# Kernel tuning notes

Measured on AMD Instinct MI355X. Metric: run time of the kernel, lower is better.

The kernel has to match this reference:

```python
import jax, jax.numpy as jnp
import numpy as np

INPUT_SIZE = 4
SEQ = 256
EMB = 64
QKV = 64
BATCH = 64
INDICES = np.array([0, 0, 1, 1])
BLK = SEQ // INPUT_SIZE                      # 64 positions per block
POS_GROUP = np.repeat(INDICES, BLK)          # per-position group id, shape [SEQ]
NUM_HEADS = len(np.unique(INDICES))          # 2
GROUP_POS = [np.where(POS_GROUP == g)[0] for g in range(NUM_HEADS)]  # static index sets


def _linear_params(key, din, dout):
    # torch nn.Linear default init: U(-1/sqrt(din), 1/sqrt(din))
    kw, kb = jax.random.split(key)
    s = 1.0 / np.sqrt(din)
    W = jax.random.uniform(kw, (dout, din), jnp.float32, -s, s)
    b = jax.random.uniform(kb, (dout,), jnp.float32, -s, s)
    return W, b


def setup_inputs() -> dict:
    key = jax.random.key(0)
    keys = jax.random.split(key, 1 + 3 * NUM_HEADS)
    inp = {"x": jax.random.normal(keys[0], (BATCH, SEQ, EMB), jnp.float32)}
    for g in range(NUM_HEADS):
        L = len(GROUP_POS[g])                # 128
        din, dout = L * EMB, L * QKV         # 8192 -> 8192
        WQ, bQ = _linear_params(keys[1 + 3 * g + 0], din, dout)
        WK, bK = _linear_params(keys[1 + 3 * g + 1], din, dout)
        WV, bV = _linear_params(keys[1 + 3 * g + 2], din, dout)
        inp[f"WQ{g}"], inp[f"bQ{g}"] = WQ, bQ
        inp[f"WK{g}"], inp[f"bK{g}"] = WK, bK
        inp[f"WV{g}"], inp[f"bV{g}"] = WV, bV
    return inp


def _head(xs, WQ, bQ, WK, bK, WV, bV, L):
    # xs: [B, L*EMB] flattened group slice
    B = xs.shape[0]
    Q = (xs @ WQ.T + bQ).reshape(B, L, QKV)
    K = (xs @ WK.T + bK).reshape(B, L, QKV)
    V = (xs @ WV.T + bV).reshape(B, L, QKV)
    scores = jnp.einsum("bik,bjk->bij", Q, K)        # [B, L, L]
    # Original uses nn.Softmax(dim=1): normalize over the QUERY axis (axis=1).
    attn = jax.nn.softmax(scores, axis=1)
    Z = jnp.einsum("bij,bjk->bik", attn, V)
    # coeff applied AFTER attention @ V, as in the original
    return Z * (1.0 / jnp.sqrt(jnp.float32(QKV)))


def reference(x, WQ0, bQ0, WK0, bK0, WV0, bV0, WQ1, bQ1, WK1, bK1, WV1, bV1):
    params = [(WQ0, bQ0, WK0, bK0, WV0, bV0), (WQ1, bQ1, WK1, bK1, WV1, bV1)]
    B = x.shape[0]
    out = jnp.zeros((B, SEQ, QKV), jnp.float32)
    for g in range(NUM_HEADS):                        # small static loop over groups
        pos = GROUP_POS[g]
        L = len(pos)
        xs = x[:, pos, :].reshape(B, L * EMB)
        Z = _head(xs, *params[g], L)
        out = out.at[:, pos, :].set(Z)
    return out
```

## Files before the change

kernel.cpp:

```cpp
#include <hip/hip_runtime.h>
#include <hip/hip_bf16.h>

#define BATCH 64
#define SEQ   256
#define EMB   64
#define QKVD  64
#define KD    8192
#define ND    8192
#define SEQD  16384
#define BKT   256
#define NTK   (KD / BKT)

typedef __attribute__((ext_vector_type(8))) short bf16x8;
typedef __attribute__((ext_vector_type(4))) float f32x4;

struct WArgs { const float* W[6]; const float* b[6]; };

__device__ __forceinline__ short f2bf(float f) {
    unsigned u = __builtin_bit_cast(unsigned, f);
    u += 0x7fffu + ((u >> 16) & 1u);
    return (short)(u >> 16);
}

__device__ __forceinline__ void gl16(const void* g, void* l) {
    __builtin_amdgcn_global_load_lds(
        (const __attribute__((address_space(1))) void*)g,
        (__attribute__((address_space(3))) void*)l, 16, 0, 0);
}

__device__ __forceinline__ void barrier_fenced() {
    asm volatile("" ::: "memory");
    __builtin_amdgcn_s_barrier();
    asm volatile("" ::: "memory");
}

__global__ __launch_bounds__(256)
void cvt_x_kernel(const float* __restrict__ x, short* __restrict__ xb) {
    const int i = (blockIdx.x * 256 + threadIdx.x) * 4;
    float4 v = *reinterpret_cast<const float4*>(x + i);
    short4 o;
    o.x = f2bf(v.x); o.y = f2bf(v.y); o.z = f2bf(v.z); o.w = f2bf(v.w);
    *reinterpret_cast<short4*>(xb + i) = o;
}

__global__ __launch_bounds__(256, 2)
void qkv_gemm_kernel(const short* __restrict__ xb, WArgs wa,
                     float* __restrict__ qkv) {
    __shared__ __attribute__((aligned(16))) float W_lds[2][32 * BKT];
    __shared__ __attribute__((aligned(16))) short A_lds[32 * BKT];

    const int wv  = threadIdx.x >> 6;
    const int ln  = threadIdx.x & 63;
    const int r   = ln & 15;
    const int kb  = ln >> 4;
    const int key = r & 7;
    const int mq  = wv & 1;
    const int nq  = wv >> 1;

    const int bid = blockIdx.x;
    const int xcd = bid & 7;
    const int q   = bid >> 3;
    const int mh  = q & 1;
    const int p   = xcd * 192 + (q >> 1);
    const int gi  = p >> 8;
    const int n0  = (p & 255) * 32;
    const int g   = gi / 3;
    const int m0  = mh * 32;

    const char*  __restrict__ Wb8 =
        (const char*)(wa.W[gi] + (size_t)n0 * KD);
    const short* __restrict__ Ag = xb + g * KD;

    f32x4 acc = {0.f, 0.f, 0.f, 0.f};

    auto stageW = [&](int t, int slot) {
        const char* tb = Wb8 + (size_t)t * 1024;
        #pragma unroll
        for (int i = 0; i < 8; ++i) {
            const int row = wv * 8 + i;
            gl16(tb + (size_t)row * (KD * 4) + ((ln ^ (row & 7)) << 4),
                 (char*)&W_lds[slot][0] + row * 1024);
        }
    };
    auto stageA = [&](int t) {
        #pragma unroll
        for (int j = 0; j < 4; ++j) {
            const int jj  = wv * 4 + j;
            const int row = 2 * jj + (ln >> 5);
            const int c   = (ln & 31) ^ (row & 7);
            gl16((const char*)(Ag + (size_t)(m0 + row) * SEQD)
                     + (size_t)t * 512 + (c << 4),
                 (char*)&A_lds[0] + jj * 1024);
        }
    };

    auto compute = [&](int slot) {
        const float* Wrow = &W_lds[slot][0] + (nq * 16 + r) * BKT;
        const char*  Ab   = (const char*)&A_lds[0] + (mq * 16 + r) * 512;
        #pragma unroll
        for (int s = 0; s < 8; ++s) {
            const int cg = s * 8 + kb * 2;
            f32x4 w0 = *(const f32x4*)(Wrow + (((cg)     ^ key) << 2));
            f32x4 w1 = *(const f32x4*)(Wrow + (((cg + 1) ^ key) << 2));
            bf16x8 bb;
            bb[0] = f2bf(w0[0]); bb[1] = f2bf(w0[1]);
            bb[2] = f2bf(w0[2]); bb[3] = f2bf(w0[3]);
            bb[4] = f2bf(w1[0]); bb[5] = f2bf(w1[1]);
            bb[6] = f2bf(w1[2]); bb[7] = f2bf(w1[3]);
            const int ca = (s * 4 + kb) ^ key;
            const bf16x8 a = *(const bf16x8*)(Ab + (ca << 4));
            acc = __builtin_amdgcn_mfma_f32_16x16x32_bf16(a, bb, acc, 0, 0, 0);
        }
    };

    stageW(0, 0);
    stageA(0);
    stageW(1, 1);

    for (int t = 0; t < NTK; ++t) {
        if (t < NTK - 1) { asm volatile("s_waitcnt vmcnt(8)" ::: "memory"); }
        else             { asm volatile("s_waitcnt vmcnt(0)" ::: "memory"); }
        __builtin_amdgcn_sched_barrier(0);
        barrier_fenced();
        compute(t & 1);
        barrier_fenced();
        if (t + 1 < NTK) stageA(t + 1);
        if (t + 2 < NTK) stageW(t + 2, t & 1);
    }

    const int nbr = n0 + nq * 16 + r;
    const float bias = wa.b[gi][nbr];
    float* orow = qkv + (size_t)gi * (BATCH * ND) + nbr;
    #pragma unroll
    for (int reg = 0; reg < 4; ++reg) {
        const int m = m0 + mq * 16 + kb * 4 + reg;
        orow[(size_t)m * ND] = acc[reg] + bias;
    }
}

__global__ __launch_bounds__(256)
void attn_kernel(const float* __restrict__ qkv, float* __restrict__ out) {
    __shared__ float Ql[128 * 65];
    __shared__ float Kl[128 * 65];
    __shared__ float Sc[128 * 129];
    __shared__ float Pm[256];
    __shared__ float Ps[256];
    __shared__ float Rden[128];

    const int b = blockIdx.x;
    const int g = blockIdx.y;
    const int t = threadIdx.x;

    const float* __restrict__ Qg = qkv + ((size_t)(3 * g + 0) * BATCH + b) * ND;
    const float* __restrict__ Kg = qkv + ((size_t)(3 * g + 1) * BATCH + b) * ND;
    const float* __restrict__ Vg = qkv + ((size_t)(3 * g + 2) * BATCH + b) * ND;

    for (int e = t; e < 8192; e += 256) {
        const int i = e >> 6, k = e & 63;
        Ql[i * 65 + k] = Qg[e];
        Kl[i * 65 + k] = Kg[e];
    }
    __syncthreads();

    {
        const int i0 = (t >> 4) * 8;
        const int j0 = (t & 15) * 8;
        float s[8][8];
        #pragma unroll
        for (int rr = 0; rr < 8; ++rr)
            #pragma unroll
            for (int cc = 0; cc < 8; ++cc) s[rr][cc] = 0.f;
        for (int k = 0; k < 64; ++k) {
            float qv[8], kv[8];
            #pragma unroll
            for (int rr = 0; rr < 8; ++rr) qv[rr] = Ql[(i0 + rr) * 65 + k];
            #pragma unroll
            for (int cc = 0; cc < 8; ++cc) kv[cc] = Kl[(j0 + cc) * 65 + k];
            #pragma unroll
            for (int rr = 0; rr < 8; ++rr)
                #pragma unroll
                for (int cc = 0; cc < 8; ++cc)
                    s[rr][cc] = fmaf(qv[rr], kv[cc], s[rr][cc]);
        }
        #pragma unroll
        for (int rr = 0; rr < 8; ++rr)
            #pragma unroll
            for (int cc = 0; cc < 8; ++cc)
                Sc[(i0 + rr) * 129 + (j0 + cc)] = s[rr][cc];
    }
    __syncthreads();

    const int j = t & 127, h = t >> 7;
    {
        for (int e = t; e < 8192; e += 256) {
            const int i = e >> 6, k = e & 63;
            Ql[i * 65 + k] = Vg[e];
        }
        float m = -3.0e38f;
        for (int i = h * 64; i < h * 64 + 64; ++i)
            m = fmaxf(m, Sc[i * 129 + j]);
        Pm[h * 128 + j] = m;
    }
    __syncthreads();
    {
        const float m = fmaxf(Pm[j], Pm[128 + j]);
        float sum = 0.f;
        for (int i = h * 64; i < h * 64 + 64; ++i) {
            const float e = __expf(Sc[i * 129 + j] - m);
            Sc[i * 129 + j] = e;
            sum += e;
        }
        Ps[h * 128 + j] = sum;
    }
    __syncthreads();
    if (t < 128) Rden[t] = 1.0f / (Ps[t] + Ps[128 + t]);
    __syncthreads();

    {
        const int i0 = (t >> 4) * 8;
        const int k0 = (t & 15) * 4;
        float z[8][4];
        #pragma unroll
        for (int rr = 0; rr < 8; ++rr)
            #pragma unroll
            for (int cc = 0; cc < 4; ++cc) z[rr][cc] = 0.f;
        for (int jj = 0; jj < 128; ++jj) {
            const float rd = Rden[jj];
            float av[8], vv[4];
            #pragma unroll
            for (int rr = 0; rr < 8; ++rr) av[rr] = Sc[(i0 + rr) * 129 + jj] * rd;
            #pragma unroll
            for (int cc = 0; cc < 4; ++cc) vv[cc] = Ql[jj * 65 + k0 + cc];
            #pragma unroll
            for (int rr = 0; rr < 8; ++rr)
                #pragma unroll
                for (int cc = 0; cc < 4; ++cc)
                    z[rr][cc] = fmaf(av[rr], vv[cc], z[rr][cc]);
        }
        float* op = out + (size_t)b * (SEQ * QKVD) + (size_t)(g * 128) * QKVD + k0;
        #pragma unroll
        for (int rr = 0; rr < 8; ++rr) {
            float4 o;
            o.x = z[rr][0] * 0.125f; o.y = z[rr][1] * 0.125f;
            o.z = z[rr][2] * 0.125f; o.w = z[rr][3] * 0.125f;
            *reinterpret_cast<float4*>(op + (size_t)(i0 + rr) * QKVD) = o;
        }
    }
}

extern "C" void kernel_launch(void* const* d_in, const int* in_sizes, int n_in,
                              void* d_out, int out_size, void* d_ws, size_t ws_size,
                              hipStream_t stream) {
    const float* x = (const float*)d_in[0];
    WArgs wa;
    for (int g = 0; g < 2; ++g)
        for (int q = 0; q < 3; ++q) {
            wa.W[g * 3 + q] = (const float*)d_in[1 + g * 6 + q * 2];
            wa.b[g * 3 + q] = (const float*)d_in[2 + g * 6 + q * 2];
        }

    short* xb  = (short*)d_ws;
    float* qkv = (float*)((char*)d_ws + (size_t)4 * 1024 * 1024);

    cvt_x_kernel<<<dim3(1024), dim3(256), 0, stream>>>(x, xb);
    qkv_gemm_kernel<<<dim3(3072), dim3(256), 0, stream>>>(xb, wa, qkv);
    attn_kernel<<<dim3(BATCH, 2), dim3(256), 0, stream>>>(qkv, (float*)d_out);
}
```

Before: 401.6 us.

## Make QKV GEMM persistent with 16-column subtiles and full-M blocks

Replaces the 3072-block GEMM grid with 256 persistent blocks that each loop over 12 sixteen-column output subtiles, covering all 64 batch rows per block and doubling the K tile to 512. Each weight element is now fetched by exactly one block, aiming to cut duplicated weight traffic and launch tail effects. In exchange the activation tile is reloaded from global for every K step, occupancy drops to one block per CU, and the existing wait counts may no longer match the load counts.

After: 553.0 us. 37.7% more time.

```diff
diff --git a/kernel.cpp b/kernel.cpp
--- a/kernel.cpp
+++ b/kernel.cpp
@@ -8,8 +8,9 @@
 #define KD    8192
 #define ND    8192
 #define SEQD  16384
-#define BKT   256
-#define NTK   (KD / BKT)
+#define BKT   512
+#define NSUB  12
+#define NTOT  (NSUB * 16)
 
 typedef __attribute__((ext_vector_type(8))) short bf16x8;
 typedef __attribute__((ext_vector_type(4))) float f32x4;
@@ -43,98 +44,107 @@
     *reinterpret_cast<short4*>(xb + i) = o;
 }
 
-__global__ __launch_bounds__(256, 2)
+__global__ __launch_bounds__(256, 1)
 void qkv_gemm_kernel(const short* __restrict__ xb, WArgs wa,
                      float* __restrict__ qkv) {
-    __shared__ __attribute__((aligned(16))) float W_lds[2][32 * BKT];
-    __shared__ __attribute__((aligned(16))) short A_lds[32 * BKT];
+    __shared__ __attribute__((aligned(16))) float W_lds[2][16 * BKT];
+    __shared__ __attribute__((aligned(16))) short A_lds[64 * BKT];
 
     const int wv  = threadIdx.x >> 6;
     const int ln  = threadIdx.x & 63;
     const int r   = ln & 15;
     const int kb  = ln >> 4;
     const int key = r & 7;
-    const int mq  = wv & 1;
-    const int nq  = wv >> 1;
-
-    const int bid = blockIdx.x;
-    const int xcd = bid & 7;
-    const int q   = bid >> 3;
-    const int mh  = q & 1;
-    const int p   = xcd * 192 + (q >> 1);
-    const int gi  = p >> 8;
-    const int n0  = (p & 255) * 32;
-    const int g   = gi / 3;
-    const int m0  = mh * 32;
-
-    const char*  __restrict__ Wb8 =
-        (const char*)(wa.W[gi] + (size_t)n0 * KD);
-    const short* __restrict__ Ag = xb + g * KD;
+
+    const int bid  = blockIdx.x;
+    const int xcd  = bid & 7;
+    const int idx  = bid >> 3;
+    const int lbase = (xcd & 1) * 1536 + ((xcd >> 1) * 32 + idx) * NSUB;
 
     f32x4 acc = {0.f, 0.f, 0.f, 0.f};
 
-    auto stageW = [&](int t, int slot) {
-        const char* tb = Wb8 + (size_t)t * 1024;
-        #pragma unroll
-        for (int i = 0; i < 8; ++i) {
-            const int row = wv * 8 + i;
-            gl16(tb + (size_t)row * (KD * 4) + ((ln ^ (row & 7)) << 4),
-                 (char*)&W_lds[slot][0] + row * 1024);
-        }
-    };
-    auto stageA = [&](int t) {
-        #pragma unroll
-        for (int j = 0; j < 4; ++j) {
-            const int jj  = wv * 4 + j;
-            const int row = 2 * jj + (ln >> 5);
-            const int c   = (ln & 31) ^ (row & 7);
-            gl16((const char*)(Ag + (size_t)(m0 + row) * SEQD)
-                     + (size_t)t * 512 + (c << 4),
-                 (char*)&A_lds[0] + jj * 1024);
-        }
-    };
-
-    auto compute = [&](int slot) {
-        const float* Wrow = &W_lds[slot][0] + (nq * 16 + r) * BKT;
-        const char*  Ab   = (const char*)&A_lds[0] + (mq * 16 + r) * 512;
-        #pragma unroll
-        for (int s = 0; s < 8; ++s) {
-            const int cg = s * 8 + kb * 2;
-            f32x4 w0 = *(const f32x4*)(Wrow + (((cg)     ^ key) << 2));
-            f32x4 w1 = *(const f32x4*)(Wrow + (((cg + 1) ^ key) << 2));
+    auto stageW = [&](int tau) {
+        if (tau >= NTOT) return;
+        const int logical = lbase + (tau >> 4);
+        const int gi_ = logical >> 9;
+        const int n0_ = (logical & 511) * 16;
+        const char* Wp = (const char*)wa.W[gi_];
+        float* slot = &W_lds[tau & 1][0];
+        #pragma unroll
+        for (int i = 0; i < 4; ++i) {
+            const int row = wv * 4 + i;
+            const size_t base =
+                ((size_t)(n0_ + row) * KD + (size_t)(tau & 15) * BKT) * 4;
+            #pragma unroll
+            for (int j = 0; j < 2; ++j)
+                gl16(Wp + base + j * 1024 + ((ln ^ (row & 7)) << 4),
+                     (char*)slot + row * 2048 + j * 1024);
+        }
+    };
+
+    auto stageA = [&](int tau) {
+        if (tau >= NTOT) return;
+        const int logical = lbase + (tau >> 4);
+        const int g_ = (logical >> 9) / 3;
+        const char* Ap = (const char*)(xb + (size_t)g_ * KD);
+        #pragma unroll
+        for (int i = 0; i < 16; ++i) {
+            const int row = wv * 16 + i;
+            gl16(Ap + ((size_t)row * SEQD + (size_t)(tau & 15) * BKT) * 2
+                     + ((ln ^ (row & 7)) << 4),
+                 (char*)&A_lds[0] + row * 1024);
+        }
+    };
+
+    auto compute = [&](int tau) {
+        const float* Wrow  = &W_lds[tau & 1][0] + r * BKT;
+        const char*  Abase = (const char*)&A_lds[0] + (wv * 16 + r) * 1024;
+        #pragma unroll
+        for (int s = 0; s < 16; ++s) {
+            const int half = s >> 3;
+            const int c0   = (s & 7) * 8 + kb * 2;
+            f32x4 w0 = *(const f32x4*)(Wrow + half * 256 + (((c0)     ^ key) << 2));
+            f32x4 w1 = *(const f32x4*)(Wrow + half * 256 + (((c0 + 1) ^ key) << 2));
             bf16x8 bb;
             bb[0] = f2bf(w0[0]); bb[1] = f2bf(w0[1]);
             bb[2] = f2bf(w0[2]); bb[3] = f2bf(w0[3]);
             bb[4] = f2bf(w1[0]); bb[5] = f2bf(w1[1]);
             bb[6] = f2bf(w1[2]); bb[7] = f2bf(w1[3]);
             const int ca = (s * 4 + kb) ^ key;
-            const bf16x8 a = *(const bf16x8*)(Ab + (ca << 4));
+            const bf16x8 a = *(const bf16x8*)(Abase + (ca << 4));
             acc = __builtin_amdgcn_mfma_f32_16x16x32_bf16(a, bb, acc, 0, 0, 0);
         }
     };
 
-    stageW(0, 0);
+    auto epilogue = [&](int sub) {
+        const int logical = lbase + sub;
+        const int gi_ = logical >> 9;
+        const int n0_ = (logical & 511) * 16;
+        const int nbr = n0_ + r;
+        const float bias = wa.b[gi_][nbr];
+        float* orow = qkv + (size_t)gi_ * (BATCH * ND) + nbr;
+        #pragma unroll
+        for (int reg = 0; reg < 4; ++reg) {
+            const int m = wv * 16 + kb * 4 + reg;
+            orow[(size_t)m * ND] = acc[reg] + bias;
+        }
+        acc[0] = 0.f; acc[1] = 0.f; acc[2] = 0.f; acc[3] = 0.f;
+    };
+
+    stageW(0);
     stageA(0);
-    stageW(1, 1);
-
-    for (int t = 0; t < NTK; ++t) {
-        if (t < NTK - 1) { asm volatile("s_waitcnt vmcnt(8)" ::: "memory"); }
-        else             { asm volatile("s_waitcnt vmcnt(0)" ::: "memory"); }
+    stageW(1);
+
+    for (int tau = 0; tau < NTOT; ++tau) {
+        if (tau < NTOT - 1) { asm volatile("s_waitcnt vmcnt(8)" ::: "memory"); }
+        else                { asm volatile("s_waitcnt vmcnt(0)" ::: "memory"); }
         __builtin_amdgcn_sched_barrier(0);
         barrier_fenced();
-        compute(t & 1);
+        compute(tau);
+        if ((tau & 15) == 15) epilogue(tau >> 4);
         barrier_fenced();
-        if (t + 1 < NTK) stageA(t + 1);
-        if (t + 2 < NTK) stageW(t + 2, t & 1);
-    }
-
-    const int nbr = n0 + nq * 16 + r;
-    const float bias = wa.b[gi][nbr];
-    float* orow = qkv + (size_t)gi * (BATCH * ND) + nbr;
-    #pragma unroll
-    for (int reg = 0; reg < 4; ++reg) {
-        const int m = m0 + mq * 16 + kb * 4 + reg;
-        orow[(size_t)m * ND] = acc[reg] + bias;
+        stageA(tau + 1);
+        stageW(tau + 2);
     }
 }
 
@@ -263,6 +273,6 @@
     float* qkv = (float*)((char*)d_ws + (size_t)4 * 1024 * 1024);
 
     cvt_x_kernel<<<dim3(1024), dim3(256), 0, stream>>>(x, xb);
-    qkv_gemm_kernel<<<dim3(3072), dim3(256), 0, stream>>>(xb, wa, qkv);
+    qkv_gemm_kernel<<<dim3(256), dim3(256), 0, stream>>>(xb, wa, qkv);
     attn_kernel<<<dim3(BATCH, 2), dim3(256), 0, stream>>>(qkv, (float*)d_out);
 }
```
